# Optimization experiments

Hardware: AMD Instinct MI355X
Metric: run time of the kernel (lower is better)

Reference implementation:

```python
import jax, jax.numpy as jnp
import numpy as np


def setup_inputs() -> dict:
    key = jax.random.key(0)
    B, N, C, H, W = 2, 512, 256, 128, 224
    ks = jax.random.split(key, 6)
    point_features = jax.random.normal(ks[0], (B, N, C), dtype=jnp.float32)
    gd = jax.random.uniform(ks[1], (B, N, 14), dtype=jnp.float32)
    # realistic radar positions (meters): X in [-10,10], Y in [-2,2], Z (depth) in [1,41]
    pos = jnp.stack([(gd[..., 0] - 0.5) * 20.0,
                     (gd[..., 1] - 0.5) * 4.0,
                     gd[..., 2] * 40.0 + 1.0], axis=-1)
    gd = gd.at[..., :3].set(pos)
    # sigmas in original-image pixels, in [0, 20] so some exceed 1 after scaling
    gd = gd.at[..., 5:7].set(gd[..., 5:7] * 20.0)
    # nuScenes-like intrinsics for a 1600x900 camera
    K = jnp.array([[500.0, 0.0, 800.0], [0.0, 500.0, 450.0], [0.0, 0.0, 1.0]], dtype=jnp.float32)
    intrinsic = jnp.tile(K[None], (B, 1, 1))
    sc = 1.0 / np.sqrt(C)
    W1 = jax.random.normal(ks[2], (C, C), dtype=jnp.float32) * sc
    b1 = jax.random.normal(ks[3], (C,), dtype=jnp.float32) * 0.01
    W2 = jax.random.normal(ks[4], (C, C), dtype=jnp.float32) * sc
    b2 = jax.random.normal(ks[5], (C,), dtype=jnp.float32) * 0.01
    return {"point_features": point_features, "gaussian_data": gd, "intrinsic": intrinsic,
            "W1": W1, "b1": b1, "W2": W2, "b2": b2, "H": H, "W": W}


def reference(point_features, gaussian_data, intrinsic, W1, b1, W2, b2, H, W):
    pf, gd, K = point_features, gaussian_data, intrinsic
    B, N, C = pf.shape
    # positions / sigmas are consumed via numpy/.item() in the original -> constants w.r.t. autodiff
    pos = jax.lax.stop_gradient(gd[..., :3])          # (B,N,3)
    sig_x = jax.lax.stop_gradient(gd[..., 5])         # (B,N)
    sig_y = jax.lax.stop_gradient(gd[..., 6])         # (B,N)
    wts = gd[..., 12]                                  # (B,N) differentiable weights

    valid = pos[..., 2] > 0.1
    # project to image plane
    p2h = jnp.einsum('bij,bnj->bni', K, pos)           # (B,N,3)
    p2 = p2h[..., :2] / (p2h[..., 2:3] + 1e-6)
    scale_x = W / K[:, 0, 2] / 2.0                     # (B,)
    scale_y = H / K[:, 1, 2] / 2.0
    cx = p2[..., 0] * scale_x[:, None]                 # (B,N)
    cy = p2[..., 1] * scale_y[:, None]
    inb = (cx >= 0) & (cx < W) & (cy >= 0) & (cy < H)
    active = (valid & inb).astype(pf.dtype)            # (B,N)

    sxv = jnp.maximum(sig_x * scale_x[:, None], 1.0)   # (B,N)
    syv = jnp.maximum(sig_y * scale_y[:, None], 1.0)

    xs = jnp.arange(W, dtype=pf.dtype)
    ys = jnp.arange(H, dtype=pf.dtype)
    dist_x = ((xs[None, None, :] - cx[..., None]) / sxv[..., None]) ** 2  # (B,N,W)
    dist_y = ((ys[None, None, :] - cy[..., None]) / syv[..., None]) ** 2  # (B,N,H)
    dist = dist_y[..., :, None] + dist_x[..., None, :]                    # (B,N,H,W)
    gw = jnp.exp(-0.5 * dist) * (dist < 9.0).astype(pf.dtype)
    gw = gw * (wts * active)[..., None, None]                             # masked splat weights

    # feature transform: Linear -> ReLU -> Linear
    h = jax.nn.relu(pf @ W1.T + b1) @ W2.T + b2                           # (B,N,C)

    feature_map = jnp.einsum('bnhw,bnc->bchw', gw, h)                     # (B,C,H,W)
    avg_sigma = 0.5 * (sxv + syv)                                         # (B,N)
    uncertainty_map = jnp.einsum('bnhw,bn->bhw', gw, avg_sigma)[:, None]  # (B,1,H,W)
    density_map = jnp.clip(jnp.sum(gw, axis=1), 1e-6, None)[:, None]      # (B,1,H,W)

    return feature_map / density_map, uncertainty_map / density_map, density_map
```

## Files before the change

kernel.cpp:

```cpp
#include <hip/hip_runtime.h>
#include <math.h>

#define MAXN 1024
#define PTS 4
#define PX 16
#define CH 16

__global__ void prep_kernel(const float* __restrict__ gd,
                            const float* __restrict__ Kmat,
                            float4* __restrict__ bbox,
                            float4* __restrict__ prm,
                            int N, int B, float Wf, float Hf) {
  int i = blockIdx.x * blockDim.x + threadIdx.x;
  if (i >= B * N) return;
  int b = i / N;
  const float* g = gd + (size_t)i * 14;
  float X = g[0], Y = g[1], Z = g[2];
  float sigx = g[5], sigy = g[6], wt = g[12];
  const float* K = Kmat + (size_t)b * 9;
  float p0 = K[0]*X + K[1]*Y + K[2]*Z;
  float p1 = K[3]*X + K[4]*Y + K[5]*Z;
  float p2 = K[6]*X + K[7]*Y + K[8]*Z;
  float denom = p2 + 1e-6f;
  float p2x = p0 / denom, p2y = p1 / denom;
  float scale_x = Wf / K[2] * 0.5f;
  float scale_y = Hf / K[5] * 0.5f;
  float cx = p2x * scale_x;
  float cy = p2y * scale_y;
  bool valid = Z > 0.1f;
  bool inb = (cx >= 0.f) && (cx < Wf) && (cy >= 0.f) && (cy < Hf);
  bool active = valid && inb;
  float sxv = fmaxf(sigx * scale_x, 1.f);
  float syv = fmaxf(sigy * scale_y, 1.f);
  float wn = active ? wt : 0.f;
  float avg = 0.5f * (sxv + syv);
  if (active && wn != 0.f) {
    bbox[i] = make_float4(cx, cy, 3.f * sxv, 3.f * syv);
  } else {
    bbox[i] = make_float4(-1e30f, -1e30f, 0.f, 0.f);
  }
  prm[i] = make_float4(1.f / sxv, 1.f / syv, wn, avg);
}

__global__ __launch_bounds__(256) void mlp_kernel(
    const float* __restrict__ pf, const float* __restrict__ W1,
    const float* __restrict__ b1, const float* __restrict__ W2,
    const float* __restrict__ b2, float* __restrict__ hout, int npts) {
  const int t = threadIdx.x;
  const int p0 = blockIdx.x * PTS;
  __shared__ __align__(16) float xs[PTS][256];

  const float4* pf4 = (const float4*)(pf + (size_t)p0 * 256);
  float4* xs4 = (float4*)&xs[0][0];
  #pragma unroll
  for (int i = 0; i < PTS * 64 / 256; ++i) xs4[t + 256 * i] = pf4[t + 256 * i];
  __syncthreads();

  float acc[PTS];
  float bb1 = b1[t];
  #pragma unroll
  for (int p = 0; p < PTS; ++p) acc[p] = bb1;
  const float* w1r = W1 + (size_t)t * 256;
  for (int k = 0; k < 256; k += 4) {
    float4 w = *(const float4*)(w1r + k);
    #pragma unroll
    for (int p = 0; p < PTS; ++p) {
      float4 x = *(const float4*)(&xs[p][k]);
      acc[p] += w.x * x.x + w.y * x.y + w.z * x.z + w.w * x.w;
    }
  }
  __syncthreads();
  #pragma unroll
  for (int p = 0; p < PTS; ++p) xs[p][t] = fmaxf(acc[p], 0.f);
  __syncthreads();

  float acc2[PTS];
  float bb2 = b2[t];
  #pragma unroll
  for (int p = 0; p < PTS; ++p) acc2[p] = bb2;
  const float* w2r = W2 + (size_t)t * 256;
  for (int k = 0; k < 256; k += 4) {
    float4 w = *(const float4*)(w2r + k);
    #pragma unroll
    for (int p = 0; p < PTS; ++p) {
      float4 x = *(const float4*)(&xs[p][k]);
      acc2[p] += w.x * x.x + w.y * x.y + w.z * x.z + w.w * x.w;
    }
  }
  #pragma unroll
  for (int p = 0; p < PTS; ++p)
    if (p0 + p < npts) hout[((size_t)(p0 + p)) * 256 + t] = acc2[p];
}

__global__ __launch_bounds__(256) void rowcull_kernel(
    const float4* __restrict__ bbox, unsigned short* __restrict__ rowlist,
    int* __restrict__ rowcnt, int N, int H, int W) {
  const int t = threadIdx.x;
  const int row = blockIdx.x;
  const int b = blockIdx.y;
  __shared__ int wcnt[4];
  const float rf = (float)row;
  const float wmax = (float)(W - 1);
  const int lane = t & 63, wave = t >> 6;
  const unsigned long long lmask = (1ull << lane) - 1ull;
  const size_t bN = (size_t)b * N;
  unsigned short* rl = rowlist + ((size_t)b * H + row) * N;

  int listlen = 0;
  for (int gb = 0; gb < N; gb += 256) {
    int g = gb + t;
    bool f = false;
    if (g < N) {
      float4 bb = bbox[bN + g];
      f = (bb.y - bb.w <= rf) && (bb.y + bb.w >= rf) &&
          (bb.x + bb.z >= 0.f) && (bb.x - bb.z <= wmax);
    }
    unsigned long long m = __ballot(f);
    if (lane == 0) wcnt[wave] = __popcll(m);
    __syncthreads();
    int pre = 0;
    #pragma unroll
    for (int wv = 0; wv < 4; ++wv) pre += (wv < wave) ? wcnt[wv] : 0;
    int tot = wcnt[0] + wcnt[1] + wcnt[2] + wcnt[3];
    if (f) rl[listlen + pre + __popcll(m & lmask)] = (unsigned short)g;
    __syncthreads();
    listlen += tot;
  }
  if (t == 0) rowcnt[(size_t)b * H + row] = listlen;
}

__global__ __launch_bounds__(256, 4) void splat_kernel(
    const float4* __restrict__ bbox, const float4* __restrict__ prm,
    const float* __restrict__ hfeat,
    const unsigned short* __restrict__ rowlist, const int* __restrict__ rowcnt,
    float* __restrict__ fout, float* __restrict__ unc_out,
    float* __restrict__ dens_out, int N, int C, int H, int W) {
  const int t = threadIdx.x;
  const int b = blockIdx.z;
  const int row = blockIdx.y;
  const int x0 = blockIdx.x * PX;
  const int HW = H * W;

  __shared__ int glist[512];
  __shared__ int wcnt[4];
  __shared__ __align__(16) float wlds[CH][PX];
  __shared__ __align__(16) float invd_s[PX];
  __shared__ float avgs_s[CH];

  const float rf = (float)row;
  const float xlo = (float)x0, xhi = (float)(x0 + PX - 1);
  const int lane = t & 63, wave = t >> 6;
  const unsigned long long lmask = (1ull << lane) - 1ull;
  const size_t bN = (size_t)b * N;
  const int rcnt = rowcnt[(size_t)b * H + row];
  const unsigned short* rl = rowlist + ((size_t)b * H + row) * N;

  int listlen = 0;
  for (int rb = 0; rb < rcnt; rb += 256) {
    int g = 0;
    bool f = false;
    if (rb + t < rcnt) {
      g = rl[rb + t];
      float4 bb = bbox[bN + g];
      f = (bb.x + bb.z >= xlo) && (bb.x - bb.z <= xhi);
    }
    unsigned long long m = __ballot(f);
    if (lane == 0) wcnt[wave] = __popcll(m);
    __syncthreads();
    int pre = 0;
    #pragma unroll
    for (int wv = 0; wv < 4; ++wv) pre += (wv < wave) ? wcnt[wv] : 0;
    int tot = wcnt[0] + wcnt[1] + wcnt[2] + wcnt[3];
    if (f) glist[listlen + pre + __popcll(m & lmask)] = g;
    __syncthreads();
    listlen += tot;
  }

  float dreg = 0.f, ureg = 0.f;
  float acc[PX];
  #pragma unroll
  for (int j = 0; j < PX; ++j) acc[j] = 0.f;

  for (int cb = 0; cb < listlen; cb += CH) {
    int gc = min(CH, listlen - cb);
    if (t < gc * PX) {
      int gi = t >> 4, j = t & 15;
      int g = glist[cb + gi];
      float4 bb = bbox[bN + g];
      float4 pr = prm[bN + g];
      float dx = (xlo + (float)j - bb.x) * pr.x;
      float dy = (rf - bb.y) * pr.y;
      float q = dx * dx + dy * dy;
      float w = (q < 9.f) ? __expf(-0.5f * q) * pr.z : 0.f;
      wlds[gi][j] = w;
      if (j == 0) avgs_s[gi] = pr.w;
    }
    __syncthreads();
    if (t < PX) {
      for (int gi = 0; gi < gc; ++gi) {
        float w = wlds[gi][t];
        dreg += w;
        ureg += w * avgs_s[gi];
      }
    }
    for (int gi = 0; gi < gc; ++gi) {
      float hv = hfeat[(bN + glist[cb + gi]) * (size_t)C + t];
      const float4* wr = (const float4*)&wlds[gi][0];
      float4 w0 = wr[0], w1 = wr[1], w2 = wr[2], w3 = wr[3];
      acc[0]  += w0.x * hv; acc[1]  += w0.y * hv; acc[2]  += w0.z * hv; acc[3]  += w0.w * hv;
      acc[4]  += w1.x * hv; acc[5]  += w1.y * hv; acc[6]  += w1.z * hv; acc[7]  += w1.w * hv;
      acc[8]  += w2.x * hv; acc[9]  += w2.y * hv; acc[10] += w2.z * hv; acc[11] += w2.w * hv;
      acc[12] += w3.x * hv; acc[13] += w3.y * hv; acc[14] += w3.z * hv; acc[15] += w3.w * hv;
    }
    __syncthreads();
  }

  if (t < PX) {
    float dc = fmaxf(dreg, 1e-6f);
    float inv = 1.f / dc;
    invd_s[t] = inv;
    size_t pix = (size_t)b * HW + (size_t)row * W + x0 + t;
    dens_out[pix] = dc;
    unc_out[pix] = ureg * inv;
  }
  __syncthreads();

  float* fo = fout + ((size_t)(b * C + t)) * HW + (size_t)row * W + x0;
  const float4* iv = (const float4*)invd_s;
  float4 i0 = iv[0], i1 = iv[1], i2 = iv[2], i3 = iv[3];
  *(float4*)(fo)      = make_float4(acc[0]*i0.x,  acc[1]*i0.y,  acc[2]*i0.z,  acc[3]*i0.w);
  *(float4*)(fo + 4)  = make_float4(acc[4]*i1.x,  acc[5]*i1.y,  acc[6]*i1.z,  acc[7]*i1.w);
  *(float4*)(fo + 8)  = make_float4(acc[8]*i2.x,  acc[9]*i2.y,  acc[10]*i2.z, acc[11]*i2.w);
  *(float4*)(fo + 12) = make_float4(acc[12]*i3.x, acc[13]*i3.y, acc[14]*i3.z, acc[15]*i3.w);
}

extern "C" void kernel_launch(void* const* d_in, const int* in_sizes, int n_in,
                              void* d_out, int out_size, void* d_ws, size_t ws_size,
                              hipStream_t stream) {
  const float* pf = (const float*)d_in[0];
  const float* gd = (const float*)d_in[1];
  const float* K  = (const float*)d_in[2];
  const float* W1 = (const float*)d_in[3];
  const float* b1 = (const float*)d_in[4];
  const float* W2 = (const float*)d_in[5];
  const float* b2 = (const float*)d_in[6];

  const int B = in_sizes[2] / 9;
  const int N = in_sizes[1] / (B * 14);
  const int C = in_sizes[0] / (B * N);
  const int H = 128, W = 224;

  float4* bbox = (float4*)d_ws;
  float4* prm  = bbox + (size_t)B * N;
  float*  hfe  = (float*)(prm + (size_t)B * N);
  unsigned short* rowlist = (unsigned short*)(hfe + (size_t)B * N * C);
  int* rowcnt = (int*)(rowlist + (size_t)B * H * N);

  float* out      = (float*)d_out;
  float* unc_out  = out + (size_t)B * C * H * W;
  float* dens_out = unc_out + (size_t)B * H * W;

  prep_kernel<<<dim3((B * N + 255) / 256), 256, 0, stream>>>(
      gd, K, bbox, prm, N, B, (float)W, (float)H);
  mlp_kernel<<<dim3((B * N + PTS - 1) / PTS), 256, 0, stream>>>(
      pf, W1, b1, W2, b2, hfe, B * N);
  rowcull_kernel<<<dim3(H, B), 256, 0, stream>>>(
      bbox, rowlist, rowcnt, N, H, W);
  splat_kernel<<<dim3(W / PX, H, B), 256, 0, stream>>>(
      bbox, prm, hfe, rowlist, rowcnt, out, unc_out, dens_out, N, C, H, W);
}
```

Before: 83.07 us.

## Double-buffer splat weights and prefetch per-chunk features before the barrier

The splat loop now double-buffers the per-chunk weight and sigma tiles in shared memory, which removes the second __syncthreads per chunk. Each thread issues all of its feature loads for the chunk up front, before the weight computation and barrier, so global-load latency overlaps the exp and bbox work. The accumulate loop is fully unrolled, with a fixed first half and a conditional second half, and weights for missing points are zero-filled. The cost is more registers for the 16 prefetched values and twice the shared memory for the weights, which may lower occupancy under launch_bounds(256,4).

After: 79.26 us. 1.05x faster.

```diff
diff --git a/kernel.cpp b/kernel.cpp
--- a/kernel.cpp
+++ b/kernel.cpp
@@ -1,7 +1,6 @@
 #include <hip/hip_runtime.h>
 #include <math.h>
 
-#define MAXN 1024
 #define PTS 4
 #define PX 16
 #define CH 16
@@ -143,9 +142,9 @@
 
   __shared__ int glist[512];
   __shared__ int wcnt[4];
-  __shared__ __align__(16) float wlds[CH][PX];
+  __shared__ __align__(16) float wlds[2][CH][PX];
   __shared__ __align__(16) float invd_s[PX];
-  __shared__ float avgs_s[CH];
+  __shared__ float avgs_s[2][CH];
 
   const float rf = (float)row;
   const float xlo = (float)x0, xhi = (float)(x0 + PX - 1);
@@ -181,38 +180,67 @@
   #pragma unroll
   for (int j = 0; j < PX; ++j) acc[j] = 0.f;
 
-  for (int cb = 0; cb < listlen; cb += CH) {
-    int gc = min(CH, listlen - cb);
-    if (t < gc * PX) {
-      int gi = t >> 4, j = t & 15;
-      int g = glist[cb + gi];
-      float4 bb = bbox[bN + g];
-      float4 pr = prm[bN + g];
-      float dx = (xlo + (float)j - bb.x) * pr.x;
-      float dy = (rf - bb.y) * pr.y;
-      float q = dx * dx + dy * dy;
-      float w = (q < 9.f) ? __expf(-0.5f * q) * pr.z : 0.f;
-      wlds[gi][j] = w;
-      if (j == 0) avgs_s[gi] = pr.w;
-    }
-    __syncthreads();
+  const int gi_w = t >> 4, j_w = t & 15;
+
+  const int nchunk = (listlen + CH - 1) / CH;
+  for (int c = 0; c < nchunk; ++c) {
+    const int cb = c * CH;
+    const int buf = c & 1;
+    const int gc = min(CH, listlen - cb);
+
+    float hvv[CH];
+    #pragma unroll
+    for (int gi = 0; gi < CH; ++gi) {
+      if (gi < gc) hvv[gi] = hfeat[(bN + glist[cb + gi]) * (size_t)C + t];
+      else         hvv[gi] = 0.f;
+    }
+
+    {
+      float w = 0.f, av = 0.f;
+      if (gi_w < gc) {
+        int g = glist[cb + gi_w];
+        float4 bb = bbox[bN + g];
+        float4 pr = prm[bN + g];
+        float dx = (xlo + (float)j_w - bb.x) * pr.x;
+        float dy = (rf - bb.y) * pr.y;
+        float q = dx * dx + dy * dy;
+        w = (q < 9.f) ? __expf(-0.5f * q) * pr.z : 0.f;
+        av = pr.w;
+      }
+      wlds[buf][gi_w][j_w] = w;
+      if (j_w == 0) avgs_s[buf][gi_w] = av;
+    }
+    __syncthreads();
+
     if (t < PX) {
       for (int gi = 0; gi < gc; ++gi) {
-        float w = wlds[gi][t];
+        float w = wlds[buf][gi][t];
         dreg += w;
-        ureg += w * avgs_s[gi];
+        ureg += w * avgs_s[buf][gi];
       }
     }
-    for (int gi = 0; gi < gc; ++gi) {
-      float hv = hfeat[(bN + glist[cb + gi]) * (size_t)C + t];
-      const float4* wr = (const float4*)&wlds[gi][0];
-      float4 w0 = wr[0], w1 = wr[1], w2 = wr[2], w3 = wr[3];
-      acc[0]  += w0.x * hv; acc[1]  += w0.y * hv; acc[2]  += w0.z * hv; acc[3]  += w0.w * hv;
-      acc[4]  += w1.x * hv; acc[5]  += w1.y * hv; acc[6]  += w1.z * hv; acc[7]  += w1.w * hv;
-      acc[8]  += w2.x * hv; acc[9]  += w2.y * hv; acc[10] += w2.z * hv; acc[11] += w2.w * hv;
-      acc[12] += w3.x * hv; acc[13] += w3.y * hv; acc[14] += w3.z * hv; acc[15] += w3.w * hv;
-    }
-    __syncthreads();
+
+    const float4* wr = (const float4*)&wlds[buf][0][0];
+    #pragma unroll
+    for (int gi = 0; gi < 8; ++gi) {
+      float4 w0 = wr[gi*4+0], w1 = wr[gi*4+1], w2 = wr[gi*4+2], w3 = wr[gi*4+3];
+      float hv = hvv[gi];
+      acc[0]  += w0.x*hv; acc[1]  += w0.y*hv; acc[2]  += w0.z*hv; acc[3]  += w0.w*hv;
+      acc[4]  += w1.x*hv; acc[5]  += w1.y*hv; acc[6]  += w1.z*hv; acc[7]  += w1.w*hv;
+      acc[8]  += w2.x*hv; acc[9]  += w2.y*hv; acc[10] += w2.z*hv; acc[11] += w2.w*hv;
+      acc[12] += w3.x*hv; acc[13] += w3.y*hv; acc[14] += w3.z*hv; acc[15] += w3.w*hv;
+    }
+    if (gc > 8) {
+      #pragma unroll
+      for (int gi = 8; gi < CH; ++gi) {
+        float4 w0 = wr[gi*4+0], w1 = wr[gi*4+1], w2 = wr[gi*4+2], w3 = wr[gi*4+3];
+        float hv = hvv[gi];
+        acc[0]  += w0.x*hv; acc[1]  += w0.y*hv; acc[2]  += w0.z*hv; acc[3]  += w0.w*hv;
+        acc[4]  += w1.x*hv; acc[5]  += w1.y*hv; acc[6]  += w1.z*hv; acc[7]  += w1.w*hv;
+        acc[8]  += w2.x*hv; acc[9]  += w2.y*hv; acc[10] += w2.z*hv; acc[11] += w2.w*hv;
+        acc[12] += w3.x*hv; acc[13] += w3.y*hv; acc[14] += w3.z*hv; acc[15] += w3.w*hv;
+      }
+    }
   }
 
   if (t < PX) {
```

## Precompute per-tile point lists and double-buffer weight/feature loads in splat

Applied to the files above, without the earlier changes.

Per-tile culling moves out of the splat kernel and into the row-cull kernel, which now writes one compact point list per 16-pixel tile, so splat blocks just copy their list instead of each running a ballot compaction. The splat loop is software-pipelined with double-buffered weight tiles and register-prefetched feature values, so the next chunk's loads overlap the current chunk's FMAs. The MLP processes more points per block with a changed launch bound. The serial per-tile scan over up to 14 threads in the cull kernel, the larger workspace, and the extra registers for the prefetch buffers could reduce occupancy.

After: 131.9 us. 58.8% more time.

```diff
diff --git a/kernel.cpp b/kernel.cpp
--- a/kernel.cpp
+++ b/kernel.cpp
@@ -1,10 +1,11 @@
 #include <hip/hip_runtime.h>
 #include <math.h>
 
-#define MAXN 1024
-#define PTS 4
+#define PTS 8
 #define PX 16
 #define CH 16
+#define NTX 14
+#define TCAP 512
 
 __global__ void prep_kernel(const float* __restrict__ gd,
                             const float* __restrict__ Kmat,
@@ -42,7 +43,7 @@
   prm[i] = make_float4(1.f / sxv, 1.f / syv, wn, avg);
 }
 
-__global__ __launch_bounds__(256) void mlp_kernel(
+__global__ __launch_bounds__(256, 2) void mlp_kernel(
     const float* __restrict__ pf, const float* __restrict__ W1,
     const float* __restrict__ b1, const float* __restrict__ W2,
     const float* __restrict__ b2, float* __restrict__ hout, int npts) {
@@ -92,21 +93,23 @@
     if (p0 + p < npts) hout[((size_t)(p0 + p)) * 256 + t] = acc2[p];
 }
 
-__global__ __launch_bounds__(256) void rowcull_kernel(
-    const float4* __restrict__ bbox, unsigned short* __restrict__ rowlist,
-    int* __restrict__ rowcnt, int N, int H, int W) {
+__global__ __launch_bounds__(256) void tilecull_kernel(
+    const float4* __restrict__ bbox, unsigned short* __restrict__ tilelist,
+    int* __restrict__ tilecnt, int N, int H, int W) {
   const int t = threadIdx.x;
   const int row = blockIdx.x;
   const int b = blockIdx.y;
+  __shared__ int rowg[512];
+  __shared__ unsigned short tl[NTX][TCAP];
+  __shared__ int tcnt[NTX];
   __shared__ int wcnt[4];
   const float rf = (float)row;
   const float wmax = (float)(W - 1);
   const int lane = t & 63, wave = t >> 6;
   const unsigned long long lmask = (1ull << lane) - 1ull;
   const size_t bN = (size_t)b * N;
-  unsigned short* rl = rowlist + ((size_t)b * H + row) * N;
-
-  int listlen = 0;
+
+  int rowlen = 0;
   for (int gb = 0; gb < N; gb += 256) {
     int g = gb + t;
     bool f = false;
@@ -122,97 +125,133 @@
     #pragma unroll
     for (int wv = 0; wv < 4; ++wv) pre += (wv < wave) ? wcnt[wv] : 0;
     int tot = wcnt[0] + wcnt[1] + wcnt[2] + wcnt[3];
-    if (f) rl[listlen + pre + __popcll(m & lmask)] = (unsigned short)g;
+    if (f) rowg[rowlen + pre + __popcll(m & lmask)] = g;
     __syncthreads();
-    listlen += tot;
-  }
-  if (t == 0) rowcnt[(size_t)b * H + row] = listlen;
-}
-
-__global__ __launch_bounds__(256, 4) void splat_kernel(
+    rowlen += tot;
+  }
+
+  if (t < NTX) {
+    const float txlo = (float)(t * PX), txhi = (float)(t * PX + PX - 1);
+    int c = 0;
+    for (int i = 0; i < rowlen; ++i) {
+      int g = rowg[i];
+      float4 bb = bbox[bN + g];
+      if (bb.x + bb.z >= txlo && bb.x - bb.z <= txhi)
+        tl[t][c++] = (unsigned short)g;
+    }
+    tcnt[t] = c;
+  }
+  __syncthreads();
+
+  const size_t rbase = ((size_t)b * H + row) * NTX;
+  for (int tx = 0; tx < NTX; ++tx) {
+    int c = tcnt[tx];
+    for (int i = t; i < c; i += 256)
+      tilelist[(rbase + tx) * TCAP + i] = tl[tx][i];
+  }
+  if (t < NTX) tilecnt[rbase + t] = tcnt[t];
+}
+
+__global__ __launch_bounds__(256) void splat_kernel(
     const float4* __restrict__ bbox, const float4* __restrict__ prm,
     const float* __restrict__ hfeat,
-    const unsigned short* __restrict__ rowlist, const int* __restrict__ rowcnt,
+    const unsigned short* __restrict__ tilelist, const int* __restrict__ tilecnt,
     float* __restrict__ fout, float* __restrict__ unc_out,
     float* __restrict__ dens_out, int N, int C, int H, int W) {
   const int t = threadIdx.x;
   const int b = blockIdx.z;
   const int row = blockIdx.y;
-  const int x0 = blockIdx.x * PX;
+  const int tx = blockIdx.x;
+  const int x0 = tx * PX;
   const int HW = H * W;
 
-  __shared__ int glist[512];
-  __shared__ int wcnt[4];
-  __shared__ __align__(16) float wlds[CH][PX];
+  __shared__ int glist[TCAP];
+  __shared__ __align__(16) float wlds[2][CH][PX];
   __shared__ __align__(16) float invd_s[PX];
-  __shared__ float avgs_s[CH];
+  __shared__ float avgs_s[2][CH];
 
   const float rf = (float)row;
-  const float xlo = (float)x0, xhi = (float)(x0 + PX - 1);
-  const int lane = t & 63, wave = t >> 6;
-  const unsigned long long lmask = (1ull << lane) - 1ull;
+  const float xlo = (float)x0;
   const size_t bN = (size_t)b * N;
-  const int rcnt = rowcnt[(size_t)b * H + row];
-  const unsigned short* rl = rowlist + ((size_t)b * H + row) * N;
-
-  int listlen = 0;
-  for (int rb = 0; rb < rcnt; rb += 256) {
-    int g = 0;
-    bool f = false;
-    if (rb + t < rcnt) {
-      g = rl[rb + t];
-      float4 bb = bbox[bN + g];
-      f = (bb.x + bb.z >= xlo) && (bb.x - bb.z <= xhi);
-    }
-    unsigned long long m = __ballot(f);
-    if (lane == 0) wcnt[wave] = __popcll(m);
-    __syncthreads();
-    int pre = 0;
-    #pragma unroll
-    for (int wv = 0; wv < 4; ++wv) pre += (wv < wave) ? wcnt[wv] : 0;
-    int tot = wcnt[0] + wcnt[1] + wcnt[2] + wcnt[3];
-    if (f) glist[listlen + pre + __popcll(m & lmask)] = g;
-    __syncthreads();
-    listlen += tot;
-  }
+  const size_t tbase = ((size_t)b * H + row) * NTX + tx;
+  const int cnt = tilecnt[tbase];
+  const unsigned short* rl = tilelist + tbase * TCAP;
+
+  for (int i = t; i < cnt; i += 256) glist[i] = rl[i];
+  __syncthreads();
 
   float dreg = 0.f, ureg = 0.f;
   float acc[PX];
   #pragma unroll
   for (int j = 0; j < PX; ++j) acc[j] = 0.f;
 
-  for (int cb = 0; cb < listlen; cb += CH) {
-    int gc = min(CH, listlen - cb);
-    if (t < gc * PX) {
-      int gi = t >> 4, j = t & 15;
-      int g = glist[cb + gi];
-      float4 bb = bbox[bN + g];
-      float4 pr = prm[bN + g];
-      float dx = (xlo + (float)j - bb.x) * pr.x;
-      float dy = (rf - bb.y) * pr.y;
-      float q = dx * dx + dy * dy;
-      float w = (q < 9.f) ? __expf(-0.5f * q) * pr.z : 0.f;
-      wlds[gi][j] = w;
-      if (j == 0) avgs_s[gi] = pr.w;
-    }
+  const int gi_w = t >> 4, j_w = t & 15;
+  const int nchunk = (cnt + CH - 1) / CH;
+
+  float hvA[CH], hvB[CH];
+
+#define WEIGHTS(BUF, CB) do { \
+    float w_ = 0.f, av_ = 0.f; \
+    int gcw_ = cnt - (CB); \
+    if (gi_w < gcw_) { \
+      int g_ = glist[(CB) + gi_w]; \
+      float4 bb_ = bbox[bN + g_]; \
+      float4 pr_ = prm[bN + g_]; \
+      float dx_ = (xlo + (float)j_w - bb_.x) * pr_.x; \
+      float dy_ = (rf - bb_.y) * pr_.y; \
+      float q_ = dx_ * dx_ + dy_ * dy_; \
+      w_ = (q_ < 9.f) ? __expf(-0.5f * q_) * pr_.z : 0.f; \
+      av_ = pr_.w; \
+    } \
+    wlds[BUF][gi_w][j_w] = w_; \
+    if (j_w == 0) avgs_s[BUF][gi_w] = av_; \
+  } while (0)
+
+#define HVLOAD(HV, CB) do { \
+    int gch_ = cnt - (CB); \
+    _Pragma("unroll") \
+    for (int gi = 0; gi < CH; ++gi) \
+      HV[gi] = (gi < gch_) ? hfeat[(bN + glist[(CB) + gi]) * (size_t)C + t] : 0.f; \
+  } while (0)
+
+#define FMAHALF(WR, HV, LO, HI) do { \
+    _Pragma("unroll") \
+    for (int gi = (LO); gi < (HI); ++gi) { \
+      float4 w0 = WR[gi*4+0], w1 = WR[gi*4+1], w2 = WR[gi*4+2], w3 = WR[gi*4+3]; \
+      float hv = HV[gi]; \
+      acc[0]  += w0.x*hv; acc[1]  += w0.y*hv; acc[2]  += w0.z*hv; acc[3]  += w0.w*hv; \
+      acc[4]  += w1.x*hv; acc[5]  += w1.y*hv; acc[6]  += w1.z*hv; acc[7]  += w1.w*hv; \
+      acc[8]  += w2.x*hv; acc[9]  += w2.y*hv; acc[10] += w2.z*hv; acc[11] += w2.w*hv; \
+      acc[12] += w3.x*hv; acc[13] += w3.y*hv; acc[14] += w3.z*hv; acc[15] += w3.w*hv; \
+    } \
+  } while (0)
+
+#define STEP(BUF, HVC, HVN, CCUR) do { \
+    const int cb_ = (CCUR) * CH; \
+    const int gc_ = min(CH, cnt - cb_); \
+    HVLOAD(HVN, cb_ + CH); \
+    WEIGHTS(BUF ^ 1, cb_ + CH); \
+    if (t < PX) { \
+      for (int gi = 0; gi < gc_; ++gi) { \
+        float w = wlds[BUF][gi][t]; \
+        dreg += w; \
+        ureg += w * avgs_s[BUF][gi]; \
+      } \
+    } \
+    { const float4* wr_ = (const float4*)&wlds[BUF][0][0]; \
+      FMAHALF(wr_, HVC, 0, 8); \
+      if (gc_ > 8) FMAHALF(wr_, HVC, 8, CH); } \
+    __syncthreads(); \
+  } while (0)
+
+  if (nchunk > 0) {
+    HVLOAD(hvA, 0);
+    WEIGHTS(0, 0);
     __syncthreads();
-    if (t < PX) {
-      for (int gi = 0; gi < gc; ++gi) {
-        float w = wlds[gi][t];
-        dreg += w;
-        ureg += w * avgs_s[gi];
-      }
-    }
-    for (int gi = 0; gi < gc; ++gi) {
-      float hv = hfeat[(bN + glist[cb + gi]) * (size_t)C + t];
-      const float4* wr = (const float4*)&wlds[gi][0];
-      float4 w0 = wr[0], w1 = wr[1], w2 = wr[2], w3 = wr[3];
-      acc[0]  += w0.x * hv; acc[1]  += w0.y * hv; acc[2]  += w0.z * hv; acc[3]  += w0.w * hv;
-      acc[4]  += w1.x * hv; acc[5]  += w1.y * hv; acc[6]  += w1.z * hv; acc[7]  += w1.w * hv;
-      acc[8]  += w2.x * hv; acc[9]  += w2.y * hv; acc[10] += w2.z * hv; acc[11] += w2.w * hv;
-      acc[12] += w3.x * hv; acc[13] += w3.y * hv; acc[14] += w3.z * hv; acc[15] += w3.w * hv;
-    }
-    __syncthreads();
+    for (int c = 0; c < nchunk; c += 2) {
+      STEP(0, hvA, hvB, c);
+      if (c + 1 < nchunk) STEP(1, hvB, hvA, c + 1);
+    }
   }
 
   if (t < PX) {
@@ -253,8 +292,8 @@
   float4* bbox = (float4*)d_ws;
   float4* prm  = bbox + (size_t)B * N;
   float*  hfe  = (float*)(prm + (size_t)B * N);
-  unsigned short* rowlist = (unsigned short*)(hfe + (size_t)B * N * C);
-  int* rowcnt = (int*)(rowlist + (size_t)B * H * N);
+  unsigned short* tilelist = (unsigned short*)(hfe + (size_t)B * N * C);
+  int* tilecnt = (int*)(tilelist + (size_t)B * H * NTX * TCAP);
 
   float* out      = (float*)d_out;
   float* unc_out  = out + (size_t)B * C * H * W;
@@ -264,8 +303,8 @@
       gd, K, bbox, prm, N, B, (float)W, (float)H);
   mlp_kernel<<<dim3((B * N + PTS - 1) / PTS), 256, 0, stream>>>(
       pf, W1, b1, W2, b2, hfe, B * N);
-  rowcull_kernel<<<dim3(H, B), 256, 0, stream>>>(
-      bbox, rowlist, rowcnt, N, H, W);
-  splat_kernel<<<dim3(W / PX, H, B), 256, 0, stream>>>(
-      bbox, prm, hfe, rowlist, rowcnt, out, unc_out, dens_out, N, C, H, W);
-}
+  tilecull_kernel<<<dim3(H, B), 256, 0, stream>>>(
+      bbox, tilelist, tilecnt, N, H, W);
+  splat_kernel<<<dim3(NTX, H, B), 256, 0, stream>>>(
+      bbox, prm, hfe, tilelist, tilecnt, out, unc_out, dens_out, N, C, H, W);
+}
```

## Restructure splat kernel to process half-rows with per-tile lists and double buffering

Applied to the files above, without the earlier changes.

The splat kernel now runs one block per half row covering seven 16-pixel tiles. Per-gaussian row data is staged once in shared memory, and one thread per tile builds that tile's gaussian list. Each thread computes a 4-channel by 4-pixel register tile, and feature loads plus weight computation for the next chunk are double-buffered behind the FMA work. This is meant to cut the repeated culling and per-tile launch overhead of the old 14-tiles-per-row grid and to raise arithmetic reuse, but it launches far fewer blocks, builds the tile lists serially, and uses large shared and register footprints. It also changes the MLP to 8 points per block with a 2-block occupancy hint and reorders the kernel launches.

New measurement: 134.6 us. 1.62x slower.

```diff
diff --git a/kernel.cpp b/kernel.cpp
--- a/kernel.cpp
+++ b/kernel.cpp
@@ -1,10 +1,11 @@
 #include <hip/hip_runtime.h>
 #include <math.h>
 
-#define MAXN 1024
-#define PTS 4
+#define PTS 8
 #define PX 16
-#define CH 16
+#define CH 8
+#define NT 7
+#define HPX 112
 
 __global__ void prep_kernel(const float* __restrict__ gd,
                             const float* __restrict__ Kmat,
@@ -42,7 +43,7 @@
   prm[i] = make_float4(1.f / sxv, 1.f / syv, wn, avg);
 }
 
-__global__ __launch_bounds__(256) void mlp_kernel(
+__global__ __launch_bounds__(256, 2) void mlp_kernel(
     const float* __restrict__ pf, const float* __restrict__ W1,
     const float* __restrict__ b1, const float* __restrict__ W2,
     const float* __restrict__ b2, float* __restrict__ hout, int npts) {
@@ -129,7 +130,7 @@
   if (t == 0) rowcnt[(size_t)b * H + row] = listlen;
 }
 
-__global__ __launch_bounds__(256, 4) void splat_kernel(
+__global__ __launch_bounds__(256) void splatrow_kernel(
     const float4* __restrict__ bbox, const float4* __restrict__ prm,
     const float* __restrict__ hfeat,
     const unsigned short* __restrict__ rowlist, const int* __restrict__ rowcnt,
@@ -138,100 +139,151 @@
   const int t = threadIdx.x;
   const int b = blockIdx.z;
   const int row = blockIdx.y;
-  const int x0 = blockIdx.x * PX;
+  const int half = blockIdx.x;
   const int HW = H * W;
 
-  __shared__ int glist[512];
-  __shared__ int wcnt[4];
-  __shared__ __align__(16) float wlds[CH][PX];
+  __shared__ __align__(16) float4 A_s[512];
+  __shared__ __align__(16) float4 B_s[512];
+  __shared__ unsigned int tl[NT][512];
+  __shared__ int tcnt[NT];
+  __shared__ __align__(16) float wlds[2][CH][PX];
+  __shared__ float avgs_s[2][CH];
   __shared__ __align__(16) float invd_s[PX];
-  __shared__ float avgs_s[CH];
 
   const float rf = (float)row;
-  const float xlo = (float)x0, xhi = (float)(x0 + PX - 1);
-  const int lane = t & 63, wave = t >> 6;
-  const unsigned long long lmask = (1ull << lane) - 1ull;
   const size_t bN = (size_t)b * N;
   const int rcnt = rowcnt[(size_t)b * H + row];
   const unsigned short* rl = rowlist + ((size_t)b * H + row) * N;
 
-  int listlen = 0;
-  for (int rb = 0; rb < rcnt; rb += 256) {
-    int g = 0;
-    bool f = false;
-    if (rb + t < rcnt) {
-      g = rl[rb + t];
-      float4 bb = bbox[bN + g];
-      f = (bb.x + bb.z >= xlo) && (bb.x - bb.z <= xhi);
-    }
-    unsigned long long m = __ballot(f);
-    if (lane == 0) wcnt[wave] = __popcll(m);
+  for (int i = t; i < rcnt; i += 256) {
+    int g = rl[i];
+    float4 bb = bbox[bN + g];
+    float4 pr = prm[bN + g];
+    float dy = (rf - bb.y) * pr.y;
+    A_s[i] = make_float4(bb.x, pr.x, pr.z, pr.w);
+    B_s[i] = make_float4(dy * dy, bb.x - bb.z, bb.x + bb.z, __int_as_float(g));
+  }
+  __syncthreads();
+
+  if (t < NT) {
+    const float txlo = (float)(half * HPX + t * PX);
+    const float txhi = txlo + (float)(PX - 1);
+    int c = 0;
+    for (int i = 0; i < rcnt; ++i) {
+      float4 Bv = B_s[i];
+      if (Bv.z >= txlo && Bv.y <= txhi)
+        tl[t][c++] = ((unsigned int)__float_as_int(Bv.w) << 16) | (unsigned int)i;
+    }
+    tcnt[t] = c;
+  }
+  __syncthreads();
+
+  const int cg = t >> 2, pq = t & 3;
+  const int gi_w = t >> 4, j_w = t & 15;
+
+#define HV8(HV, CB) do { \
+    int gn_ = cnt - (CB); \
+    _Pragma("unroll") \
+    for (int gi = 0; gi < CH; ++gi) { \
+      float4 hv_ = make_float4(0.f, 0.f, 0.f, 0.f); \
+      if (gi < gn_) { \
+        unsigned int pk_ = tl[tx][(CB) + gi]; \
+        hv_ = *(const float4*)(hfeat + (bN + (pk_ >> 16)) * (size_t)C + 4 * cg); \
+      } \
+      HV[gi] = hv_; \
+    } } while (0)
+
+#define WGT8(BUF, CB) do { \
+    if (t < CH * PX) { \
+      float w_ = 0.f, av_ = 0.f; \
+      int gn_ = cnt - (CB); \
+      if (gi_w < gn_) { \
+        int i_ = (int)(tl[tx][(CB) + gi_w] & 0xffffu); \
+        float4 A_ = A_s[i_]; \
+        float dx_ = ((float)(x0 + j_w) - A_.x) * A_.y; \
+        float q_ = dx_ * dx_ + B_s[i_].x; \
+        w_ = (q_ < 9.f) ? __expf(-0.5f * q_) * A_.z : 0.f; \
+        av_ = A_.w; \
+      } \
+      wlds[BUF][gi_w][j_w] = w_; \
+      if (j_w == 0) avgs_s[BUF][gi_w] = av_; \
+    } } while (0)
+
+#define DENS8(BUF, GC) do { \
+    if (t < PX) { \
+      for (int gi = 0; gi < (GC); ++gi) { \
+        float w = wlds[BUF][gi][t]; \
+        dreg += w; ureg += w * avgs_s[BUF][gi]; \
+      } } } while (0)
+
+#define FMA8(BUF, HV) do { \
+    const float4* wr_ = (const float4*)&wlds[BUF][0][0]; \
+    _Pragma("unroll") \
+    for (int gi = 0; gi < CH; ++gi) { \
+      float4 w = wr_[gi * 4 + pq]; \
+      float4 h = HV[gi]; \
+      a0.x += w.x*h.x; a0.y += w.y*h.x; a0.z += w.z*h.x; a0.w += w.w*h.x; \
+      a1.x += w.x*h.y; a1.y += w.y*h.y; a1.z += w.z*h.y; a1.w += w.w*h.y; \
+      a2.x += w.x*h.z; a2.y += w.y*h.z; a2.z += w.z*h.z; a2.w += w.w*h.z; \
+      a3.x += w.x*h.w; a3.y += w.y*h.w; a3.z += w.z*h.w; a3.w += w.w*h.w; \
+    } } while (0)
+
+  for (int tx = 0; tx < NT; ++tx) {
+    const int x0 = half * HPX + tx * PX;
+    const int cnt = tcnt[tx];
+    const int nchunk = (cnt + CH - 1) / CH;
+
+    float dreg = 0.f, ureg = 0.f;
+    float4 a0 = make_float4(0.f, 0.f, 0.f, 0.f), a1 = a0, a2 = a0, a3 = a0;
+    float4 hvA[CH], hvB[CH];
+
+    if (nchunk > 0) {
+      HV8(hvA, 0);
+      WGT8(0, 0);
+      __syncthreads();
+      for (int c = 0; c < nchunk; c += 2) {
+        {
+          const int gc = min(CH, cnt - c * CH);
+          HV8(hvB, (c + 1) * CH);
+          WGT8(1, (c + 1) * CH);
+          DENS8(0, gc);
+          FMA8(0, hvA);
+          __syncthreads();
+        }
+        if (c + 1 < nchunk) {
+          const int gc = min(CH, cnt - (c + 1) * CH);
+          HV8(hvA, (c + 2) * CH);
+          WGT8(0, (c + 2) * CH);
+          DENS8(1, gc);
+          FMA8(1, hvB);
+          __syncthreads();
+        }
+      }
+    }
+
+    if (t < PX) {
+      float dc = fmaxf(dreg, 1e-6f);
+      float inv = 1.f / dc;
+      invd_s[t] = inv;
+      size_t pix = (size_t)b * HW + (size_t)row * W + x0 + t;
+      dens_out[pix] = dc;
+      unc_out[pix] = ureg * inv;
+    }
     __syncthreads();
-    int pre = 0;
-    #pragma unroll
-    for (int wv = 0; wv < 4; ++wv) pre += (wv < wave) ? wcnt[wv] : 0;
-    int tot = wcnt[0] + wcnt[1] + wcnt[2] + wcnt[3];
-    if (f) glist[listlen + pre + __popcll(m & lmask)] = g;
+
+    float4 iq = *(const float4*)&invd_s[4 * pq];
+    float* fo = fout + ((size_t)(b * C + 4 * cg)) * HW + (size_t)row * W + x0 + 4 * pq;
+    *(float4*)(fo)        = make_float4(a0.x*iq.x, a0.y*iq.y, a0.z*iq.z, a0.w*iq.w);
+    *(float4*)(fo + HW)   = make_float4(a1.x*iq.x, a1.y*iq.y, a1.z*iq.z, a1.w*iq.w);
+    *(float4*)(fo + 2*HW) = make_float4(a2.x*iq.x, a2.y*iq.y, a2.z*iq.z, a2.w*iq.w);
+    *(float4*)(fo + 3*HW) = make_float4(a3.x*iq.x, a3.y*iq.y, a3.z*iq.z, a3.w*iq.w);
     __syncthreads();
-    listlen += tot;
-  }
-
-  float dreg = 0.f, ureg = 0.f;
-  float acc[PX];
-  #pragma unroll
-  for (int j = 0; j < PX; ++j) acc[j] = 0.f;
-
-  for (int cb = 0; cb < listlen; cb += CH) {
-    int gc = min(CH, listlen - cb);
-    if (t < gc * PX) {
-      int gi = t >> 4, j = t & 15;
-      int g = glist[cb + gi];
-      float4 bb = bbox[bN + g];
-      float4 pr = prm[bN + g];
-      float dx = (xlo + (float)j - bb.x) * pr.x;
-      float dy = (rf - bb.y) * pr.y;
-      float q = dx * dx + dy * dy;
-      float w = (q < 9.f) ? __expf(-0.5f * q) * pr.z : 0.f;
-      wlds[gi][j] = w;
-      if (j == 0) avgs_s[gi] = pr.w;
-    }
-    __syncthreads();
-    if (t < PX) {
-      for (int gi = 0; gi < gc; ++gi) {
-        float w = wlds[gi][t];
-        dreg += w;
-        ureg += w * avgs_s[gi];
-      }
-    }
-    for (int gi = 0; gi < gc; ++gi) {
-      float hv = hfeat[(bN + glist[cb + gi]) * (size_t)C + t];
-      const float4* wr = (const float4*)&wlds[gi][0];
-      float4 w0 = wr[0], w1 = wr[1], w2 = wr[2], w3 = wr[3];
-      acc[0]  += w0.x * hv; acc[1]  += w0.y * hv; acc[2]  += w0.z * hv; acc[3]  += w0.w * hv;
-      acc[4]  += w1.x * hv; acc[5]  += w1.y * hv; acc[6]  += w1.z * hv; acc[7]  += w1.w * hv;
-      acc[8]  += w2.x * hv; acc[9]  += w2.y * hv; acc[10] += w2.z * hv; acc[11] += w2.w * hv;
-      acc[12] += w3.x * hv; acc[13] += w3.y * hv; acc[14] += w3.z * hv; acc[15] += w3.w * hv;
-    }
-    __syncthreads();
-  }
-
-  if (t < PX) {
-    float dc = fmaxf(dreg, 1e-6f);
-    float inv = 1.f / dc;
-    invd_s[t] = inv;
-    size_t pix = (size_t)b * HW + (size_t)row * W + x0 + t;
-    dens_out[pix] = dc;
-    unc_out[pix] = ureg * inv;
-  }
-  __syncthreads();
-
-  float* fo = fout + ((size_t)(b * C + t)) * HW + (size_t)row * W + x0;
-  const float4* iv = (const float4*)invd_s;
-  float4 i0 = iv[0], i1 = iv[1], i2 = iv[2], i3 = iv[3];
-  *(float4*)(fo)      = make_float4(acc[0]*i0.x,  acc[1]*i0.y,  acc[2]*i0.z,  acc[3]*i0.w);
-  *(float4*)(fo + 4)  = make_float4(acc[4]*i1.x,  acc[5]*i1.y,  acc[6]*i1.z,  acc[7]*i1.w);
-  *(float4*)(fo + 8)  = make_float4(acc[8]*i2.x,  acc[9]*i2.y,  acc[10]*i2.z, acc[11]*i2.w);
-  *(float4*)(fo + 12) = make_float4(acc[12]*i3.x, acc[13]*i3.y, acc[14]*i3.z, acc[15]*i3.w);
+  }
+
+#undef HV8
+#undef WGT8
+#undef DENS8
+#undef FMA8
 }
 
 extern "C" void kernel_launch(void* const* d_in, const int* in_sizes, int n_in,
@@ -250,11 +302,15 @@
   const int C = in_sizes[0] / (B * N);
   const int H = 128, W = 224;
 
-  float4* bbox = (float4*)d_ws;
-  float4* prm  = bbox + (size_t)B * N;
-  float*  hfe  = (float*)(prm + (size_t)B * N);
-  unsigned short* rowlist = (unsigned short*)(hfe + (size_t)B * N * C);
-  int* rowcnt = (int*)(rowlist + (size_t)B * H * N);
+  char* wsb = (char*)d_ws;
+  size_t off = 0;
+  float4* bbox = (float4*)(wsb + off); off += (size_t)B * N * sizeof(float4);
+  float4* prm  = (float4*)(wsb + off); off += (size_t)B * N * sizeof(float4);
+  float*  hfe  = (float*)(wsb + off);  off += (size_t)B * N * C * 4;
+  unsigned short* rowlist = (unsigned short*)(wsb + off);
+  off += (size_t)B * H * N * 2;
+  off = (off + 15) & ~(size_t)15;
+  int* rowcnt = (int*)(wsb + off);
 
   float* out      = (float*)d_out;
   float* unc_out  = out + (size_t)B * C * H * W;
@@ -262,10 +318,10 @@
 
   prep_kernel<<<dim3((B * N + 255) / 256), 256, 0, stream>>>(
       gd, K, bbox, prm, N, B, (float)W, (float)H);
+  rowcull_kernel<<<dim3(H, B), 256, 0, stream>>>(
+      bbox, rowlist, rowcnt, N, H, W);
   mlp_kernel<<<dim3((B * N + PTS - 1) / PTS), 256, 0, stream>>>(
       pf, W1, b1, W2, b2, hfe, B * N);
-  rowcull_kernel<<<dim3(H, B), 256, 0, stream>>>(
-      bbox, rowlist, rowcnt, N, H, W);
-  splat_kernel<<<dim3(W / PX, H, B), 256, 0, stream>>>(
+  splatrow_kernel<<<dim3(2, H, B), 256, 0, stream>>>(
       bbox, prm, hfe, rowlist, rowcnt, out, unc_out, dens_out, N, C, H, W);
 }
```
